# Kernel tuning notes

Measured on AMD Instinct MI355X. Metric: run time of the kernel, lower is better.

Reference implementation:

```python
import jax, jax.numpy as jnp
import numpy as np

N_NODES = 50000
N_EDGES = 800000
D = 128
N_REL = 4
N_GRAPHS = 128
N_CLASSES = 16


def rgcn_layer(x, W_rel, W_root, b, src, dst, edge_type):
    # Per-relation transform of all nodes: [N, R, D]
    xt = jnp.einsum('nd,rdf->nrf', x, W_rel)
    msg = xt[src, edge_type]  # [E, D] gather message per edge
    # mean aggregation per (dst, relation) pair (PyG RGCNConv aggr='mean')
    seg = dst * N_REL + edge_type
    cnt = jax.ops.segment_sum(jnp.ones((src.shape[0],), x.dtype), seg,
                              num_segments=N_NODES * N_REL)
    norm = 1.0 / jnp.maximum(cnt[seg], 1.0)
    agg = jax.ops.segment_sum(msg * norm[:, None], dst, num_segments=N_NODES)
    return agg + x @ W_root + b


def setup_inputs() -> dict:
    key = jax.random.key(0)
    ks = jax.random.split(key, 12)
    s = 1.0 / np.sqrt(D)
    inp = {
        'x': jax.random.normal(ks[0], (N_NODES, D), jnp.float32),
        'edge_index': jax.random.randint(ks[1], (2, N_EDGES), 0, N_NODES, jnp.int64),
        'edge_type': jax.random.randint(ks[2], (N_EDGES,), 0, N_REL, jnp.int64),
        'batch': jnp.sort(jax.random.randint(ks[3], (N_NODES,), 0, N_GRAPHS, jnp.int64)),
        'W_rel1': jax.random.normal(ks[4], (N_REL, D, D), jnp.float32) * s,
        'W_root1': jax.random.normal(ks[5], (D, D), jnp.float32) * s,
        'b1': jnp.zeros((D,), jnp.float32),
        'W_rel2': jax.random.normal(ks[6], (N_REL, D, D), jnp.float32) * s,
        'W_root2': jax.random.normal(ks[7], (D, D), jnp.float32) * s,
        'b2': jnp.zeros((D,), jnp.float32),
        'W_cls': jax.random.normal(ks[8], (D, N_CLASSES), jnp.float32) * s,
        'b_cls': jnp.zeros((N_CLASSES,), jnp.float32),
    }
    return inp


def reference(x, edge_index, edge_type, batch, W_rel1, W_root1, b1,
              W_rel2, W_root2, b2, W_cls, b_cls):
    src, dst = edge_index[0], edge_index[1]
    h = jax.nn.relu(rgcn_layer(x, W_rel1, W_root1, b1, src, dst, edge_type))
    h = jax.nn.relu(rgcn_layer(h, W_rel2, W_root2, b2, src, dst, edge_type))
    # global mean pool over graphs (dropout is identity: training=False)
    gsum = jax.ops.segment_sum(h, batch, num_segments=N_GRAPHS)
    gcnt = jax.ops.segment_sum(jnp.ones((h.shape[0],), h.dtype), batch,
                               num_segments=N_GRAPHS)
    g = gsum / jnp.maximum(gcnt, 1.0)[:, None]
    return g @ W_cls + b_cls
```

## Files before the change

kernel.cpp:

```cpp
#include <hip/hip_runtime.h>

#define D_DIM 128
#define N_REL 4
#define CAP 32

typedef __attribute__((ext_vector_type(8))) short bf16x8;
typedef __attribute__((ext_vector_type(4))) float f32x4;

static inline int cdiv(int a, int b) { return (a + b - 1) / b; }

__device__ inline ushort f2bf(float f) {
    union { float f; unsigned u; } v;
    v.f = f;
    unsigned r = v.u + 0x7FFFu + ((v.u >> 16) & 1u);
    return (ushort)(r >> 16);
}

__device__ inline float bf2f(ushort u) {
    union { unsigned u; float f; } v;
    v.u = (unsigned)u << 16;
    return v.f;
}

__device__ inline float uif(unsigned u) {
    union { unsigned u; float f; } v;
    v.u = u;
    return v.f;
}

#define CNT_B 391
#define CAST_B 6250
#define PACK_B 80

__global__ __launch_bounds__(256) void prep_kernel(
    const float* __restrict__ x, ushort* __restrict__ Xb,
    const int* __restrict__ src, const int* __restrict__ dst,
    const int* __restrict__ et, unsigned* __restrict__ icnt,
    int* __restrict__ esorted,
    const float* __restrict__ Wrel1, const float* __restrict__ Wroot1,
    const float* __restrict__ Wrel2, const float* __restrict__ Wroot2,
    ushort* __restrict__ Wpk1, ushort* __restrict__ Wpk2,
    int n4, int nEdges) {
    int b = blockIdx.x;
    if (b < CNT_B) {
        int e = (b * 256 + threadIdx.x) * 8;
        if (e >= nEdges) return;
        if (e + 8 <= nEdges) {
            int4 sA = *(const int4*)(src + e);
            int4 sB = *(const int4*)(src + e + 4);
            int4 dA = *(const int4*)(dst + e);
            int4 dB = *(const int4*)(dst + e + 4);
            int4 tA = *(const int4*)(et + e);
            int4 tB = *(const int4*)(et + e + 4);
            unsigned o0 = atomicAdd(&icnt[dA.x], 1u << (8 * tA.x));
            unsigned o1 = atomicAdd(&icnt[dA.y], 1u << (8 * tA.y));
            unsigned o2 = atomicAdd(&icnt[dA.z], 1u << (8 * tA.z));
            unsigned o3 = atomicAdd(&icnt[dA.w], 1u << (8 * tA.w));
            unsigned o4 = atomicAdd(&icnt[dB.x], 1u << (8 * tB.x));
            unsigned o5 = atomicAdd(&icnt[dB.y], 1u << (8 * tB.y));
            unsigned o6 = atomicAdd(&icnt[dB.z], 1u << (8 * tB.z));
            unsigned o7 = atomicAdd(&icnt[dB.w], 1u << (8 * tB.w));
            int r0 = (int)(((o0 >> (8 * tA.x)) & 0xFFu) - 0xAAu);
            int r1 = (int)(((o1 >> (8 * tA.y)) & 0xFFu) - 0xAAu);
            int r2 = (int)(((o2 >> (8 * tA.z)) & 0xFFu) - 0xAAu);
            int r3 = (int)(((o3 >> (8 * tA.w)) & 0xFFu) - 0xAAu);
            int r4 = (int)(((o4 >> (8 * tB.x)) & 0xFFu) - 0xAAu);
            int r5 = (int)(((o5 >> (8 * tB.y)) & 0xFFu) - 0xAAu);
            int r6 = (int)(((o6 >> (8 * tB.z)) & 0xFFu) - 0xAAu);
            int r7 = (int)(((o7 >> (8 * tB.w)) & 0xFFu) - 0xAAu);
            esorted[((size_t)(dA.x * N_REL + tA.x) << 5) + r0] = sA.x;
            esorted[((size_t)(dA.y * N_REL + tA.y) << 5) + r1] = sA.y;
            esorted[((size_t)(dA.z * N_REL + tA.z) << 5) + r2] = sA.z;
            esorted[((size_t)(dA.w * N_REL + tA.w) << 5) + r3] = sA.w;
            esorted[((size_t)(dB.x * N_REL + tB.x) << 5) + r4] = sB.x;
            esorted[((size_t)(dB.y * N_REL + tB.y) << 5) + r5] = sB.y;
            esorted[((size_t)(dB.z * N_REL + tB.z) << 5) + r6] = sB.z;
            esorted[((size_t)(dB.w * N_REL + tB.w) << 5) + r7] = sB.w;
        } else {
            for (int j = 0; e + j < nEdges; ++j) {
                int dd = dst[e + j], tt = et[e + j];
                unsigned o = atomicAdd(&icnt[dd], 1u << (8 * tt));
                int r = (int)(((o >> (8 * tt)) & 0xFFu) - 0xAAu);
                esorted[((size_t)(dd * N_REL + tt) << 5) + r] = src[e + j];
            }
        }
    } else if (b < CNT_B + CAST_B) {
        int i = (b - CNT_B) * 256 + threadIdx.x;
        if (i < n4) {
            float4 v = ((const float4*)x)[i];
            ushort4 o;
            o.x = f2bf(v.x); o.y = f2bf(v.y); o.z = f2bf(v.z); o.w = f2bf(v.w);
            ((ushort4*)Xb)[i] = o;
        }
    } else {
        int pb = b - (CNT_B + CAST_B);
        int layer = pb / 40;
        int rem = pb % 40;
        int mat = rem >> 3;
        int blk = rem & 7;
        const float* Wrel = layer ? Wrel2 : Wrel1;
        const float* Wroot = layer ? Wroot2 : Wroot1;
        ushort* out = layer ? Wpk2 : Wpk1;
        const float* W = (mat < N_REL) ? (Wrel + (size_t)mat * D_DIM * D_DIM) : Wroot;
        int t = blk * 256 + threadIdx.x;
        int lane = t & 63;
        int tile = t >> 6;
        int kt = tile >> 3;
        int nt = tile & 7;
        int n = nt * 16 + (lane & 15);
        int kb = kt * 32 + (lane >> 4) * 8;
        ushort* o = out + (((size_t)mat * 32 + tile) * 64 + lane) * 8;
        ushort4 lo, hi;
        lo.x = f2bf(W[(kb + 0) * D_DIM + n]);
        lo.y = f2bf(W[(kb + 1) * D_DIM + n]);
        lo.z = f2bf(W[(kb + 2) * D_DIM + n]);
        lo.w = f2bf(W[(kb + 3) * D_DIM + n]);
        hi.x = f2bf(W[(kb + 4) * D_DIM + n]);
        hi.y = f2bf(W[(kb + 5) * D_DIM + n]);
        hi.z = f2bf(W[(kb + 6) * D_DIM + n]);
        hi.w = f2bf(W[(kb + 7) * D_DIM + n]);
        *(ushort4*)(o) = lo;
        *(ushort4*)(o + 4) = hi;
    }
}

__global__ __launch_bounds__(256) void gather_kernel(
    const ushort* __restrict__ Xb, const unsigned* __restrict__ icnt,
    const int* __restrict__ esorted, ushort* __restrict__ M, int nseg) {
    __shared__ int ids[16][CAP];
    __shared__ int sids[16][CAP];
    __shared__ int sdeg[16];
    __shared__ int perm[16];
    const int tid = threadIdx.x;
    const int ql = tid & 15;
    const int qd = tid >> 4;
    const int seg0 = blockIdx.x * 16;

    if (tid < 16) {
        int seg = seg0 + tid;
        int deg = -1;
        if (seg < nseg) {
            unsigned w = icnt[seg >> 2];
            deg = (int)(((w >> ((seg & 3) * 8)) & 0xFFu) - 0xAAu);
        }
        sdeg[tid] = deg;
    }
    __syncthreads();
    if (tid < 16) {
        int myd = sdeg[tid];
        int rank = 0;
#pragma unroll
        for (int j = 0; j < 16; ++j) {
            int dj = sdeg[j];
            rank += (dj < myd || (dj == myd && j < tid)) ? 1 : 0;
        }
        perm[rank] = tid;
    }
    __syncthreads();

    const int local = perm[qd];
    const int seg = seg0 + local;
    const int deg = sdeg[local];
    if (deg < 0) return;
    uint4* mout = (uint4*)(M + (size_t)seg * D_DIM + ql * 8);
    const ushort* xb = Xb + ql * 8;
    const int* eb = esorted + ((size_t)seg << 5);
    if (deg == 0) {
        *mout = make_uint4(0u, 0u, 0u, 0u);
        return;
    }
    if (deg == 1) {
        *mout = *(const uint4*)(xb + (size_t)eb[0] * D_DIM);
        return;
    }
    for (int j = ql; j < deg; j += 16) ids[qd][j] = eb[j];
    __threadfence_block();
#pragma unroll
    for (int base = 0; base < 2; ++base) {
        int j = base * 16 + ql;
        if (j < deg) {
            int v = ids[qd][j];
            int rank = 0;
            for (int k = 0; k < deg; ++k) {
                int w = ids[qd][k];
                rank += (w < v || (w == v && k < j)) ? 1 : 0;
            }
            sids[qd][rank] = v;
        }
    }
    __threadfence_block();
    float a[8], b[8];
#pragma unroll
    for (int j = 0; j < 8; ++j) { a[j] = 0.f; b[j] = 0.f; }
    auto acc8 = [](float* acc, uint4 u) {
        acc[0] += uif(u.x << 16); acc[1] += uif(u.x & 0xFFFF0000u);
        acc[2] += uif(u.y << 16); acc[3] += uif(u.y & 0xFFFF0000u);
        acc[4] += uif(u.z << 16); acc[5] += uif(u.z & 0xFFFF0000u);
        acc[6] += uif(u.w << 16); acc[7] += uif(u.w & 0xFFFF0000u);
    };
    int e = 0;
    for (; e + 4 <= deg; e += 4) {
        int s0 = sids[qd][e];
        int s1 = sids[qd][e + 1];
        int s2 = sids[qd][e + 2];
        int s3 = sids[qd][e + 3];
        uint4 u0 = *(const uint4*)(xb + (size_t)s0 * D_DIM);
        uint4 u1 = *(const uint4*)(xb + (size_t)s1 * D_DIM);
        uint4 u2 = *(const uint4*)(xb + (size_t)s2 * D_DIM);
        uint4 u3 = *(const uint4*)(xb + (size_t)s3 * D_DIM);
        acc8(a, u0); acc8(b, u1); acc8(a, u2); acc8(b, u3);
    }
    if (e + 2 <= deg) {
        int s0 = sids[qd][e];
        int s1 = sids[qd][e + 1];
        uint4 u0 = *(const uint4*)(xb + (size_t)s0 * D_DIM);
        uint4 u1 = *(const uint4*)(xb + (size_t)s1 * D_DIM);
        acc8(a, u0); acc8(b, u1);
        e += 2;
    }
    if (e < deg) {
        uint4 u0 = *(const uint4*)(xb + (size_t)sids[qd][e] * D_DIM);
        acc8(a, u0);
    }
    float sc = 1.0f / (float)deg;
    uint4 o;
    o.x = (unsigned)f2bf((a[0] + b[0]) * sc) | ((unsigned)f2bf((a[1] + b[1]) * sc) << 16);
    o.y = (unsigned)f2bf((a[2] + b[2]) * sc) | ((unsigned)f2bf((a[3] + b[3]) * sc) << 16);
    o.z = (unsigned)f2bf((a[4] + b[4]) * sc) | ((unsigned)f2bf((a[5] + b[5]) * sc) << 16);
    o.w = (unsigned)f2bf((a[6] + b[6]) * sc) | ((unsigned)f2bf((a[7] + b[7]) * sc) << 16);
    *mout = o;
}

__global__ __launch_bounds__(256) void gemm_kernel(
    const ushort* __restrict__ M, const ushort* __restrict__ Xb,
    const ushort* __restrict__ Wpk, const float* __restrict__ bias,
    ushort* __restrict__ outb, int n_nodes) {
    const int tid = threadIdx.x;
    const int wave = tid >> 6;
    const int lane = tid & 63;
    const int m = lane & 15;
    const int q = lane >> 4;
    const int rh = wave >> 1;
    const int nh = wave & 1;
    const int r0 = blockIdx.x * 64 + rh * 32;
    const int n0 = min(r0 + m, n_nodes - 1);
    const int n1 = min(r0 + 16 + m, n_nodes - 1);

    const ushort* aM0 = M + (size_t)n0 * (N_REL * D_DIM) + q * 8;
    const ushort* aM1 = M + (size_t)n1 * (N_REL * D_DIM) + q * 8;
    const ushort* aX0 = Xb + (size_t)n0 * D_DIM + q * 8;
    const ushort* aX1 = Xb + (size_t)n1 * D_DIM + q * 8;

    f32x4 acc[2][4];
#pragma unroll
    for (int h = 0; h < 2; ++h)
#pragma unroll
        for (int j = 0; j < 4; ++j) acc[h][j] = (f32x4){0.f, 0.f, 0.f, 0.f};

    for (int phase = 0; phase < 5; ++phase) {
        const ushort* Bp = Wpk + (size_t)phase * 32 * 64 * 8;
        const ushort* ab0 = (phase < N_REL) ? (aM0 + phase * D_DIM) : aX0;
        const ushort* ab1 = (phase < N_REL) ? (aM1 + phase * D_DIM) : aX1;
#pragma unroll
        for (int kt = 0; kt < 4; ++kt) {
            bf16x8 a0 = *(const bf16x8*)(ab0 + kt * 32);
            bf16x8 a1 = *(const bf16x8*)(ab1 + kt * 32);
#pragma unroll
            for (int j = 0; j < 4; ++j) {
                int nt = nh * 4 + j;
                bf16x8 b = *(const bf16x8*)(Bp + ((size_t)(kt * 8 + nt) * 64 + lane) * 8);
                acc[0][j] = __builtin_amdgcn_mfma_f32_16x16x32_bf16(a0, b, acc[0][j], 0, 0, 0);
                acc[1][j] = __builtin_amdgcn_mfma_f32_16x16x32_bf16(a1, b, acc[1][j], 0, 0, 0);
            }
        }
    }

#pragma unroll
    for (int j = 0; j < 4; ++j) {
        int col = (nh * 4 + j) * 16 + m;
        float bv = bias[col];
#pragma unroll
        for (int h = 0; h < 2; ++h) {
#pragma unroll
            for (int r = 0; r < 4; ++r) {
                int row = r0 + h * 16 + q * 4 + r;
                if (row < n_nodes)
                    outb[(size_t)row * D_DIM + col] = f2bf(fmaxf(acc[h][j][r] + bv, 0.0f));
            }
        }
    }
}

__global__ __launch_bounds__(1024) void poolcls_kernel(
    const ushort* __restrict__ hb, const int* __restrict__ batch,
    const float* __restrict__ Wcls, const float* __restrict__ bcls,
    float* __restrict__ out, int n_nodes) {
    __shared__ float part[64][D_DIM + 1];
    __shared__ float mean[D_DIM];
    __shared__ float cpart[16][17];
    int g = blockIdx.x;
    int tid = threadIdx.x;
    int par = tid >> 4;
    int dg = (tid & 15) * 8;
    auto lb = [&](int val) {
        int lo = 0, hi = n_nodes;
        while (lo < hi) {
            int mid = (lo + hi) >> 1;
            if (batch[mid] < val) lo = mid + 1; else hi = mid;
        }
        return lo;
    };
    int lo = lb(g), hi = lb(g + 1);
    float a[8];
#pragma unroll
    for (int j = 0; j < 8; ++j) a[j] = 0.f;
    for (int nn = lo + par; nn < hi; nn += 64) {
        uint4 u = *(const uint4*)(hb + (size_t)nn * D_DIM + dg);
        a[0] += uif(u.x << 16); a[1] += uif(u.x & 0xFFFF0000u);
        a[2] += uif(u.y << 16); a[3] += uif(u.y & 0xFFFF0000u);
        a[4] += uif(u.z << 16); a[5] += uif(u.z & 0xFFFF0000u);
        a[6] += uif(u.w << 16); a[7] += uif(u.w & 0xFFFF0000u);
    }
#pragma unroll
    for (int j = 0; j < 8; ++j) part[par][dg + j] = a[j];
    __syncthreads();
    if (tid < D_DIM) {
        float s = 0.f;
#pragma unroll
        for (int j = 0; j < 64; ++j) s += part[j][tid];
        mean[tid] = s / fmaxf((float)(hi - lo), 1.0f);
    }
    __syncthreads();
    if (tid < 256) {
        int c = tid & 15, kc = tid >> 4;
        float s = 0.f;
#pragma unroll
        for (int j = 0; j < 8; ++j)
            s = fmaf(mean[kc * 8 + j], Wcls[(kc * 8 + j) * 16 + c], s);
        cpart[kc][c] = s;
    }
    __syncthreads();
    if (tid < 16) {
        float s = bcls[tid];
#pragma unroll
        for (int k = 0; k < 16; ++k) s += cpart[k][tid];
        out[g * 16 + tid] = s;
    }
}

extern "C" void kernel_launch(void* const* d_in, const int* in_sizes, int n_in,
                              void* d_out, int out_size, void* d_ws, size_t ws_size,
                              hipStream_t stream) {
    const float* x      = (const float*)d_in[0];
    const int*   ei     = (const int*)d_in[1];
    const int*   etype  = (const int*)d_in[2];
    const int*   batch  = (const int*)d_in[3];
    const float* Wrel1  = (const float*)d_in[4];
    const float* Wroot1 = (const float*)d_in[5];
    const float* b1     = (const float*)d_in[6];
    const float* Wrel2  = (const float*)d_in[7];
    const float* Wroot2 = (const float*)d_in[8];
    const float* b2     = (const float*)d_in[9];
    const float* Wcls   = (const float*)d_in[10];
    const float* bcls   = (const float*)d_in[11];
    float* out = (float*)d_out;

    const int N = in_sizes[0] / D_DIM;
    const int E = in_sizes[1] / 2;
    const int NSEG = N * N_REL;
    const int* src = ei;
    const int* dst = ei + E;

    ushort* Xb   = (ushort*)d_ws;
    ushort* h1b  = Xb + (size_t)N * D_DIM;
    ushort* h2b  = h1b + (size_t)N * D_DIM;
    ushort* M    = h2b + (size_t)N * D_DIM;
    ushort* Wpk1 = M + (size_t)N * N_REL * D_DIM;
    ushort* Wpk2 = Wpk1 + 81920;
    unsigned* icnt = (unsigned*)(Wpk2 + 81920);
    int* esorted = (int*)(icnt + N);

    prep_kernel<<<CNT_B + CAST_B + PACK_B, 256, 0, stream>>>(
        x, Xb, src, dst, etype, icnt, esorted, Wrel1, Wroot1, Wrel2, Wroot2,
        Wpk1, Wpk2, N * D_DIM / 4, E);

    gather_kernel<<<cdiv(NSEG, 16), 256, 0, stream>>>(
        Xb, icnt, esorted, M, NSEG);
    gemm_kernel<<<cdiv(N, 64), 256, 0, stream>>>(M, Xb, Wpk1, b1, h1b, N);

    gather_kernel<<<cdiv(NSEG, 16), 256, 0, stream>>>(
        h1b, icnt, esorted, M, NSEG);
    gemm_kernel<<<cdiv(N, 64), 256, 0, stream>>>(M, h1b, Wpk2, b2, h2b, N);

    poolcls_kernel<<<128, 1024, 0, stream>>>(h2b, batch, Wcls, bcls, out, N);
}
```

Before: 295.9 us.

## Fuse per-relation gather into GEMM kernel via shared-memory staging

Merges the gather and GEMM kernels into one layer kernel. Each block gathers mean-aggregated neighbor rows for 64 nodes, one relation at a time, into an LDS tile and feeds that tile straight to the MFMAs. This removes the global M buffer write and read plus a kernel launch per layer. In exchange the gather loses the degree-sorted load balancing, gets fewer blocks (N/64) for latency hiding, and adds block barriers that stall the MFMA phase until the slowest row finishes.

```diff
diff --git a/kernel.cpp b/kernel.cpp
--- a/kernel.cpp
+++ b/kernel.cpp
@@ -124,132 +124,24 @@
     }
 }
 
-__global__ __launch_bounds__(256) void gather_kernel(
+__global__ __launch_bounds__(256) void layer_kernel(
     const ushort* __restrict__ Xb, const unsigned* __restrict__ icnt,
-    const int* __restrict__ esorted, ushort* __restrict__ M, int nseg) {
-    __shared__ int ids[16][CAP];
-    __shared__ int sids[16][CAP];
-    __shared__ int sdeg[16];
-    __shared__ int perm[16];
-    const int tid = threadIdx.x;
-    const int ql = tid & 15;
-    const int qd = tid >> 4;
-    const int seg0 = blockIdx.x * 16;
-
-    if (tid < 16) {
-        int seg = seg0 + tid;
-        int deg = -1;
-        if (seg < nseg) {
-            unsigned w = icnt[seg >> 2];
-            deg = (int)(((w >> ((seg & 3) * 8)) & 0xFFu) - 0xAAu);
-        }
-        sdeg[tid] = deg;
-    }
-    __syncthreads();
-    if (tid < 16) {
-        int myd = sdeg[tid];
-        int rank = 0;
-#pragma unroll
-        for (int j = 0; j < 16; ++j) {
-            int dj = sdeg[j];
-            rank += (dj < myd || (dj == myd && j < tid)) ? 1 : 0;
-        }
-        perm[rank] = tid;
-    }
-    __syncthreads();
-
-    const int local = perm[qd];
-    const int seg = seg0 + local;
-    const int deg = sdeg[local];
-    if (deg < 0) return;
-    uint4* mout = (uint4*)(M + (size_t)seg * D_DIM + ql * 8);
-    const ushort* xb = Xb + ql * 8;
-    const int* eb = esorted + ((size_t)seg << 5);
-    if (deg == 0) {
-        *mout = make_uint4(0u, 0u, 0u, 0u);
-        return;
-    }
-    if (deg == 1) {
-        *mout = *(const uint4*)(xb + (size_t)eb[0] * D_DIM);
-        return;
-    }
-    for (int j = ql; j < deg; j += 16) ids[qd][j] = eb[j];
-    __threadfence_block();
-#pragma unroll
-    for (int base = 0; base < 2; ++base) {
-        int j = base * 16 + ql;
-        if (j < deg) {
-            int v = ids[qd][j];
-            int rank = 0;
-            for (int k = 0; k < deg; ++k) {
-                int w = ids[qd][k];
-                rank += (w < v || (w == v && k < j)) ? 1 : 0;
-            }
-            sids[qd][rank] = v;
-        }
-    }
-    __threadfence_block();
-    float a[8], b[8];
-#pragma unroll
-    for (int j = 0; j < 8; ++j) { a[j] = 0.f; b[j] = 0.f; }
-    auto acc8 = [](float* acc, uint4 u) {
-        acc[0] += uif(u.x << 16); acc[1] += uif(u.x & 0xFFFF0000u);
-        acc[2] += uif(u.y << 16); acc[3] += uif(u.y & 0xFFFF0000u);
-        acc[4] += uif(u.z << 16); acc[5] += uif(u.z & 0xFFFF0000u);
-        acc[6] += uif(u.w << 16); acc[7] += uif(u.w & 0xFFFF0000u);
-    };
-    int e = 0;
-    for (; e + 4 <= deg; e += 4) {
-        int s0 = sids[qd][e];
-        int s1 = sids[qd][e + 1];
-        int s2 = sids[qd][e + 2];
-        int s3 = sids[qd][e + 3];
-        uint4 u0 = *(const uint4*)(xb + (size_t)s0 * D_DIM);
-        uint4 u1 = *(const uint4*)(xb + (size_t)s1 * D_DIM);
-        uint4 u2 = *(const uint4*)(xb + (size_t)s2 * D_DIM);
-        uint4 u3 = *(const uint4*)(xb + (size_t)s3 * D_DIM);
-        acc8(a, u0); acc8(b, u1); acc8(a, u2); acc8(b, u3);
-    }
-    if (e + 2 <= deg) {
-        int s0 = sids[qd][e];
-        int s1 = sids[qd][e + 1];
-        uint4 u0 = *(const uint4*)(xb + (size_t)s0 * D_DIM);
-        uint4 u1 = *(const uint4*)(xb + (size_t)s1 * D_DIM);
-        acc8(a, u0); acc8(b, u1);
-        e += 2;
-    }
-    if (e < deg) {
-        uint4 u0 = *(const uint4*)(xb + (size_t)sids[qd][e] * D_DIM);
-        acc8(a, u0);
-    }
-    float sc = 1.0f / (float)deg;
-    uint4 o;
-    o.x = (unsigned)f2bf((a[0] + b[0]) * sc) | ((unsigned)f2bf((a[1] + b[1]) * sc) << 16);
-    o.y = (unsigned)f2bf((a[2] + b[2]) * sc) | ((unsigned)f2bf((a[3] + b[3]) * sc) << 16);
-    o.z = (unsigned)f2bf((a[4] + b[4]) * sc) | ((unsigned)f2bf((a[5] + b[5]) * sc) << 16);
-    o.w = (unsigned)f2bf((a[6] + b[6]) * sc) | ((unsigned)f2bf((a[7] + b[7]) * sc) << 16);
-    *mout = o;
-}
-
-__global__ __launch_bounds__(256) void gemm_kernel(
-    const ushort* __restrict__ M, const ushort* __restrict__ Xb,
-    const ushort* __restrict__ Wpk, const float* __restrict__ bias,
-    ushort* __restrict__ outb, int n_nodes) {
+    const int* __restrict__ esorted, const ushort* __restrict__ Wpk,
+    const float* __restrict__ bias, ushort* __restrict__ outb, int n_nodes) {
+    __shared__ ushort Ms[64][136];
+    __shared__ int ids[16][33];
+    __shared__ int sids[16][33];
     const int tid = threadIdx.x;
     const int wave = tid >> 6;
     const int lane = tid & 63;
+    const int ql = tid & 15;
+    const int qd = tid >> 4;
     const int m = lane & 15;
     const int q = lane >> 4;
     const int rh = wave >> 1;
     const int nh = wave & 1;
-    const int r0 = blockIdx.x * 64 + rh * 32;
-    const int n0 = min(r0 + m, n_nodes - 1);
-    const int n1 = min(r0 + 16 + m, n_nodes - 1);
-
-    const ushort* aM0 = M + (size_t)n0 * (N_REL * D_DIM) + q * 8;
-    const ushort* aM1 = M + (size_t)n1 * (N_REL * D_DIM) + q * 8;
-    const ushort* aX0 = Xb + (size_t)n0 * D_DIM + q * 8;
-    const ushort* aX1 = Xb + (size_t)n1 * D_DIM + q * 8;
+    const int r0b = blockIdx.x * 64;
+    const int r0 = r0b + rh * 32;
 
     f32x4 acc[2][4];
 #pragma unroll
@@ -257,14 +149,109 @@
 #pragma unroll
         for (int j = 0; j < 4; ++j) acc[h][j] = (f32x4){0.f, 0.f, 0.f, 0.f};
 
-    for (int phase = 0; phase < 5; ++phase) {
-        const ushort* Bp = Wpk + (size_t)phase * 32 * 64 * 8;
-        const ushort* ab0 = (phase < N_REL) ? (aM0 + phase * D_DIM) : aX0;
-        const ushort* ab1 = (phase < N_REL) ? (aM1 + phase * D_DIM) : aX1;
+    auto acc8 = [](float* a, uint4 u) {
+        a[0] += uif(u.x << 16); a[1] += uif(u.x & 0xFFFF0000u);
+        a[2] += uif(u.y << 16); a[3] += uif(u.y & 0xFFFF0000u);
+        a[4] += uif(u.z << 16); a[5] += uif(u.z & 0xFFFF0000u);
+        a[6] += uif(u.w << 16); a[7] += uif(u.w & 0xFFFF0000u);
+    };
+
+    for (int rel = 0; rel < N_REL; ++rel) {
+        for (int rr = 0; rr < 4; ++rr) {
+            const int row = rr * 16 + qd;
+            const int node = r0b + row;
+            int deg = 0;
+            if (node < n_nodes) {
+                unsigned w = icnt[node];
+                deg = (int)(((w >> (rel * 8)) & 0xFFu) - 0xAAu);
+            }
+            uint4* mrow = (uint4*)&Ms[row][ql * 8];
+            const ushort* xb = Xb + ql * 8;
+            const int* eb = esorted + ((size_t)((node << 2) + rel) << 5);
+            if (deg == 0) {
+                *mrow = make_uint4(0u, 0u, 0u, 0u);
+            } else if (deg == 1) {
+                *mrow = *(const uint4*)(xb + (size_t)eb[0] * D_DIM);
+            } else {
+                for (int j = ql; j < deg; j += 16) ids[qd][j] = eb[j];
+                __threadfence_block();
+#pragma unroll
+                for (int base = 0; base < 2; ++base) {
+                    int j = base * 16 + ql;
+                    if (j < deg) {
+                        int v = ids[qd][j];
+                        int rank = 0;
+                        for (int k = 0; k < deg; ++k) {
+                            int w = ids[qd][k];
+                            rank += (w < v || (w == v && k < j)) ? 1 : 0;
+                        }
+                        sids[qd][rank] = v;
+                    }
+                }
+                __threadfence_block();
+                float a[8], b[8];
+#pragma unroll
+                for (int j = 0; j < 8; ++j) { a[j] = 0.f; b[j] = 0.f; }
+                int e = 0;
+                for (; e + 4 <= deg; e += 4) {
+                    int s0 = sids[qd][e];
+                    int s1 = sids[qd][e + 1];
+                    int s2 = sids[qd][e + 2];
+                    int s3 = sids[qd][e + 3];
+                    uint4 u0 = *(const uint4*)(xb + (size_t)s0 * D_DIM);
+                    uint4 u1 = *(const uint4*)(xb + (size_t)s1 * D_DIM);
+                    uint4 u2 = *(const uint4*)(xb + (size_t)s2 * D_DIM);
+                    uint4 u3 = *(const uint4*)(xb + (size_t)s3 * D_DIM);
+                    acc8(a, u0); acc8(b, u1); acc8(a, u2); acc8(b, u3);
+                }
+                if (e + 2 <= deg) {
+                    int s0 = sids[qd][e];
+                    int s1 = sids[qd][e + 1];
+                    uint4 u0 = *(const uint4*)(xb + (size_t)s0 * D_DIM);
+                    uint4 u1 = *(const uint4*)(xb + (size_t)s1 * D_DIM);
+                    acc8(a, u0); acc8(b, u1);
+                    e += 2;
+                }
+                if (e < deg) {
+                    uint4 u0 = *(const uint4*)(xb + (size_t)sids[qd][e] * D_DIM);
+                    acc8(a, u0);
+                }
+                float sc = 1.0f / (float)deg;
+                uint4 o;
+                o.x = (unsigned)f2bf((a[0] + b[0]) * sc) | ((unsigned)f2bf((a[1] + b[1]) * sc) << 16);
+                o.y = (unsigned)f2bf((a[2] + b[2]) * sc) | ((unsigned)f2bf((a[3] + b[3]) * sc) << 16);
+                o.z = (unsigned)f2bf((a[4] + b[4]) * sc) | ((unsigned)f2bf((a[5] + b[5]) * sc) << 16);
+                o.w = (unsigned)f2bf((a[6] + b[6]) * sc) | ((unsigned)f2bf((a[7] + b[7]) * sc) << 16);
+                *mrow = o;
+            }
+        }
+        __syncthreads();
+        const ushort* Bp = Wpk + (size_t)rel * (32 * 64 * 8);
 #pragma unroll
         for (int kt = 0; kt < 4; ++kt) {
-            bf16x8 a0 = *(const bf16x8*)(ab0 + kt * 32);
-            bf16x8 a1 = *(const bf16x8*)(ab1 + kt * 32);
+            bf16x8 a0 = *(const bf16x8*)&Ms[rh * 32 + m][kt * 32 + q * 8];
+            bf16x8 a1 = *(const bf16x8*)&Ms[rh * 32 + 16 + m][kt * 32 + q * 8];
+#pragma unroll
+            for (int j = 0; j < 4; ++j) {
+                int nt = nh * 4 + j;
+                bf16x8 b = *(const bf16x8*)(Bp + ((size_t)(kt * 8 + nt) * 64 + lane) * 8);
+                acc[0][j] = __builtin_amdgcn_mfma_f32_16x16x32_bf16(a0, b, acc[0][j], 0, 0, 0);
+                acc[1][j] = __builtin_amdgcn_mfma_f32_16x16x32_bf16(a1, b, acc[1][j], 0, 0, 0);
+            }
+        }
+        __syncthreads();
+    }
+
+    {
+        const int n0 = min(r0 + m, n_nodes - 1);
+        const int n1 = min(r0 + 16 + m, n_nodes - 1);
+        const ushort* aX0 = Xb + (size_t)n0 * D_DIM + q * 8;
+        const ushort* aX1 = Xb + (size_t)n1 * D_DIM + q * 8;
+        const ushort* Bp = Wpk + (size_t)N_REL * (32 * 64 * 8);
+#pragma unroll
+        for (int kt = 0; kt < 4; ++kt) {
+            bf16x8 a0 = *(const bf16x8*)(aX0 + kt * 32);
+            bf16x8 a1 = *(const bf16x8*)(aX1 + kt * 32);
 #pragma unroll
             for (int j = 0; j < 4; ++j) {
                 int nt = nh * 4 + j;
@@ -367,7 +354,6 @@
 
     const int N = in_sizes[0] / D_DIM;
     const int E = in_sizes[1] / 2;
-    const int NSEG = N * N_REL;
     const int* src = ei;
     const int* dst = ei + E;
 
@@ -384,13 +370,11 @@
         x, Xb, src, dst, etype, icnt, esorted, Wrel1, Wroot1, Wrel2, Wroot2,
         Wpk1, Wpk2, N * D_DIM / 4, E);
 
-    gather_kernel<<<cdiv(NSEG, 16), 256, 0, stream>>>(
-        Xb, icnt, esorted, M, NSEG);
-    gemm_kernel<<<cdiv(N, 64), 256, 0, stream>>>(M, Xb, Wpk1, b1, h1b, N);
-
-    gather_kernel<<<cdiv(NSEG, 16), 256, 0, stream>>>(
-        h1b, icnt, esorted, M, NSEG);
-    gemm_kernel<<<cdiv(N, 64), 256, 0, stream>>>(M, h1b, Wpk2, b2, h2b, N);
+    layer_kernel<<<cdiv(N, 64), 256, 0, stream>>>(
+        Xb, icnt, esorted, Wpk1, b1, h1b, N);
+
+    layer_kernel<<<cdiv(N, 64), 256, 0, stream>>>(
+        h1b, icnt, esorted, Wpk2, b2, h2b, N);
 
     poolcls_kernel<<<128, 1024, 0, stream>>>(h2b, batch, Wcls, bcls, out, N);
 }
```

Result: slower. 382.5 us (+29.3%).
